# Performance work log

Measured on AMD Instinct MI355X. Metric: run time of the kernel, lower is better.

Reference implementation:

```python
import jax, jax.numpy as jnp
import numpy as np

B, S, HID = 2, 2048, 2048
NH, NKV, D = 32, 8, 64
M = 256          # FAVOR+ random features
CHUNK = 128      # causal chunk size
EPS = 1e-6


def setup_inputs():
    key = jax.random.key(0)
    ks = jax.random.split(key, 7)
    hidden_states = jax.random.normal(ks[0], (B, S, HID), jnp.float32)
    # RoPE tables (HF Llama style): [B, S, D]
    inv_freq = 1.0 / (10000.0 ** (jnp.arange(0, D, 2, dtype=jnp.float32) / D))
    freqs = jnp.arange(S, dtype=jnp.float32)[:, None] * inv_freq[None, :]   # [S, D/2]
    emb = jnp.concatenate([freqs, freqs], axis=-1)                          # [S, D]
    cos = jnp.broadcast_to(jnp.cos(emb)[None], (B, S, D)).astype(jnp.float32)
    sin = jnp.broadcast_to(jnp.sin(emb)[None], (B, S, D)).astype(jnp.float32)
    sc = 0.02
    Wq = jax.random.normal(ks[1], (NH * D, HID), jnp.float32) * sc
    Wk = jax.random.normal(ks[2], (NKV * D, HID), jnp.float32) * sc
    Wv = jax.random.normal(ks[3], (NKV * D, HID), jnp.float32) * sc
    Wo = jax.random.normal(ks[4], (HID, NH * D), jnp.float32) * sc
    proj = jax.random.normal(ks[5], (M, D), jnp.float32)  # FAVOR+ random projection
    return {"hidden_states": hidden_states, "cos": cos, "sin": sin,
            "Wq": Wq, "Wk": Wk, "Wv": Wv, "Wo": Wo, "proj": proj}


def rotate_half(x):
    x1, x2 = x[..., : x.shape[-1] // 2], x[..., x.shape[-1] // 2:]
    return jnp.concatenate([-x2, x1], axis=-1)


def favor_features(x, proj, is_query):
    # FAVOR+ positive softmax-kernel features: phi(x) = exp(Wx' - |x'|^2/2 - stab)/sqrt(m)
    dn = x.shape[-1] ** -0.25
    xn = x * dn                                            # data normalizer d^{-1/4}
    xp = jnp.einsum('bhsd,md->bhsm', xn, proj)             # [B,H,S,M]
    sq = 0.5 * jnp.sum(xn * xn, axis=-1, keepdims=True)
    if is_query:
        stab = jnp.max(xp, axis=-1, keepdims=True)
    else:
        stab = jnp.max(xp, axis=(-1, -2), keepdims=True)
    return (jnp.exp(xp - sq - stab) + EPS) / jnp.sqrt(jnp.asarray(M, xp.dtype))


def causal_linear_attention(phi_q, phi_k, v):
    # phi_q/phi_k: [B,H,S,M], v: [B,H,S,D]; causal chunked prefix formulation
    Bh, H, T, m = phi_q.shape
    d = v.shape[-1]
    nc = T // CHUNK
    qc = phi_q.reshape(Bh, H, nc, CHUNK, m)
    kc = phi_k.reshape(Bh, H, nc, CHUNK, m)
    vc = v.reshape(Bh, H, nc, CHUNK, d)
    # per-chunk KV state and key sums
    kv = jnp.einsum('bhscm,bhscd->bhsmd', kc, vc)          # [B,H,nc,M,D]
    kz = jnp.sum(kc, axis=3)                               # [B,H,nc,M]
    kv_pre = jnp.cumsum(kv, axis=2) - kv                   # exclusive prefix
    kz_pre = jnp.cumsum(kz, axis=2) - kz
    inter = jnp.einsum('bhscm,bhsmd->bhscd', qc, kv_pre)
    inter_z = jnp.einsum('bhscm,bhsm->bhsc', qc, kz_pre)
    # intra-chunk causal part
    mask = jnp.tril(jnp.ones((CHUNK, CHUNK), phi_q.dtype))
    scores = jnp.einsum('bhscm,bhstm->bhsct', qc, kc) * mask
    intra = jnp.einsum('bhsct,bhstd->bhscd', scores, vc)
    intra_z = jnp.sum(scores, axis=-1)
    out = (inter + intra) / (inter_z + intra_z + EPS)[..., None]
    return out.reshape(Bh, H, T, d)


def reference(hidden_states, cos, sin, Wq, Wk, Wv, Wo, proj):
    b, s, _ = hidden_states.shape
    q = (hidden_states @ Wq.T).reshape(b, s, NH, D).transpose(0, 2, 1, 3)   # [B,NH,S,D]
    k = (hidden_states @ Wk.T).reshape(b, s, NKV, D).transpose(0, 2, 1, 3)  # [B,NKV,S,D]
    v = (hidden_states @ Wv.T).reshape(b, s, NKV, D).transpose(0, 2, 1, 3)
    c, si = cos[:, None, :, :], sin[:, None, :, :]
    q = q * c + rotate_half(q) * si
    k = k * c + rotate_half(k) * si
    groups = NH // NKV
    k = jnp.repeat(k, groups, axis=1)
    v = jnp.repeat(v, groups, axis=1)
    phi_q = favor_features(q, proj, is_query=True)
    phi_k = favor_features(k, proj, is_query=False)
    attn = causal_linear_attention(phi_q, phi_k, v)                         # [B,NH,S,D]
    attn = attn.transpose(0, 2, 1, 3).reshape(b, s, NH * D)
    return attn @ Wo.T
```

## Files before the change

### kernel.cpp

```cpp
#include <hip/hip_runtime.h>
#include <hip/hip_bf16.h>

#define SEQ   2048
#define NHEAD 32
#define NKVH  8
#define DH    64
#define MFEAT 256
#define NCH   16
#define EPSF  1e-6f

typedef __hip_bfloat16 bf16;
typedef unsigned short u16;
typedef __attribute__((ext_vector_type(8))) short short8;
typedef __attribute__((ext_vector_type(4))) float f32x4;

__device__ __forceinline__ float b2f(bf16 x){ return __bfloat162float(x); }
__device__ __forceinline__ bf16  f2b(float x){ return __float2bfloat16(x); }
__device__ __forceinline__ u16   f2u(float x){ bf16 h = __float2bfloat16(x); return *reinterpret_cast<u16*>(&h); }

__device__ __forceinline__ bool probe_f32(const unsigned* __restrict__ p){
  return (p[0] & 0xFFFFu) == 0u;
}
__device__ __forceinline__ float loadIn(const void* __restrict__ ptr, size_t idx, bool f32){
  return f32 ? ((const float*)ptr)[idx] : b2f(((const bf16*)ptr)[idx]);
}

__device__ __forceinline__ void cp16(u16* lds, const u16* g){
  __builtin_amdgcn_global_load_lds((const __attribute__((address_space(1))) unsigned*)g,
      (__attribute__((address_space(3))) unsigned*)lds, 16, 0, 0);
}

#define MFMA16(a,b,c) __builtin_amdgcn_mfma_f32_16x16x32_bf16(a,b,c,0,0,0)

__global__ __launch_bounds__(256) void conv_kernel(const void* __restrict__ src,
    u16* __restrict__ dst, const unsigned* __restrict__ probe)
{
  const bool f32in = probe_f32(probe);
  size_t i = ((size_t)blockIdx.x*256 + threadIdx.x)*4;
  #pragma unroll
  for (int j=0;j<4;++j) dst[i+j] = f2u(loadIn(src, i+j, f32in));
}

__global__ __launch_bounds__(512) void gemm_mfma(const u16* __restrict__ A,
    const u16* __restrict__ W, float* __restrict__ oq, float* __restrict__ ok,
    float* __restrict__ ov, void* __restrict__ outAny, int K, int N, int mode,
    const void* __restrict__ cosg, const void* __restrict__ sing,
    const unsigned* __restrict__ probe)
{
  __shared__ __align__(16) u16 sA[3][16384];
  __shared__ __align__(16) u16 sB[3][8192];
  const int tid = threadIdx.x;
  const int lane = tid & 63, wave = tid >> 6;

  const int nbx = gridDim.x;
  const int nwg = nbx * gridDim.y;
  int id = blockIdx.y * nbx + blockIdx.x;
  int sw = id;
  if ((nwg & 7) == 0) sw = (id & 7) * (nwg >> 3) + (id >> 3);
  const int bx = sw % nbx, by = sw / nbx;
  const int c0 = bx*128, r0 = by*256;

  const int wm = wave >> 1, wn = wave & 1;
  f32x4 acc[4][4] = {};

  const int rl  = lane >> 3;
  const int swzE = ((lane & 7) ^ rl) << 3;
  const u16* gA = A + (size_t)(r0 + wave*8 + rl)*K + swzE;
  const u16* gB = W + (size_t)(c0 + wave*8 + rl)*K + swzE;
  const int aDst = wave*512;
  const int bDst = wave*512;

  const int rowA = (wm*64 + (lane&15))*64;
  const int rowB = (wn*64 + (lane&15))*64;
  const int colS = (((lane>>4)*8) ^ ((lane&7)<<3));

  const int nk = K >> 6;

  #define STAGE(buf, t) do { const int k0_ = (t)*64;                      \
    cp16(&sA[buf][aDst],         gA + k0_);                               \
    cp16(&sA[buf][aDst + 4096],  gA + (size_t)64*K  + k0_);               \
    cp16(&sA[buf][aDst + 8192],  gA + (size_t)128*K + k0_);               \
    cp16(&sA[buf][aDst + 12288], gA + (size_t)192*K + k0_);               \
    cp16(&sB[buf][bDst],         gB + k0_);                               \
    cp16(&sB[buf][bDst + 4096],  gB + (size_t)64*K  + k0_); } while(0)

  STAGE(0, 0);
  STAGE(1, 1);

  int cur = 0;
  for (int t = 0; t < nk; ++t) {
    if (t < nk-1) asm volatile("s_waitcnt vmcnt(6)" ::: "memory");
    else          asm volatile("s_waitcnt vmcnt(0)" ::: "memory");
    __builtin_amdgcn_s_barrier();
    __builtin_amdgcn_sched_barrier(0);

    if (t + 2 < nk) { int sb = cur + 2; if (sb >= 3) sb -= 3; STAGE(sb, t+2); }

    const u16* bA_ = sA[cur];
    const u16* bB_ = sB[cur];
    short8 af[4][2], bfv[4][2];
    #pragma unroll
    for (int mt=0;mt<4;++mt){
      af[mt][0] = *(const short8*)(bA_ + rowA + mt*1024 + colS);
      af[mt][1] = *(const short8*)(bA_ + rowA + mt*1024 + (colS^32));
    }
    #pragma unroll
    for (int nt=0;nt<4;++nt){
      bfv[nt][0] = *(const short8*)(bB_ + rowB + nt*1024 + colS);
      bfv[nt][1] = *(const short8*)(bB_ + rowB + nt*1024 + (colS^32));
    }
    __builtin_amdgcn_s_setprio(1);
    #pragma unroll
    for (int mt=0;mt<4;++mt)
      #pragma unroll
      for (int nt=0;nt<4;++nt){
        acc[mt][nt] = MFMA16(af[mt][0], bfv[nt][0], acc[mt][nt]);
        acc[mt][nt] = MFMA16(af[mt][1], bfv[nt][1], acc[mt][nt]);
      }
    __builtin_amdgcn_s_setprio(0);

    cur = (cur == 2) ? 0 : cur + 1;
  }
  #undef STAGE

  const int rbase = r0 + wm*64 + (lane>>4)*4;
  const int cbase = c0 + wn*64 + (lane&15);
  if (mode == 0) {
    const bool f32o = probe_f32(probe);
    #pragma unroll
    for (int mt=0;mt<4;++mt)
      #pragma unroll
      for (int nt=0;nt<4;++nt)
        #pragma unroll
        for (int rg=0;rg<4;++rg){
          int r = rbase + mt*16 + rg, c = cbase + nt*16;
          float v = acc[mt][nt][rg];
          if (f32o) ((float*)outAny)[(size_t)r*N + c] = v;
          else      ((u16*)outAny)[(size_t)r*N + c] = f2u(v);
        }
  } else {
    const bool f32in = probe_f32(probe);
    const float dn = 0.3535533905932738f;
    #pragma unroll
    for (int nt=0;nt<4;++nt){
      int cc = cbase + nt*16;
      float* dst; int H2, cl; bool isv = false;
      if (cc < 2048){ dst = oq; H2 = 32; cl = cc; }
      else if (cc < 2560){ dst = ok; H2 = 8; cl = cc - 2048; }
      else { dst = ov; H2 = 8; cl = cc - 2560; isv = true; }
      int hh = cl>>6, dd = cl&63;
      float sgn = (dd < 32) ? -1.f : 1.f;
      #pragma unroll
      for (int mt=0;mt<4;++mt)
        #pragma unroll
        for (int rg=0;rg<4;++rg){
          int r = rbase + mt*16 + rg;
          int bb = r>>11, s = r&2047;
          float v = acc[mt][nt][rg];
          if (!isv){
            float vp = acc[mt][nt^2][rg];
            size_t ci = ((size_t)bb*SEQ + s)*DH + dd;
            float cv = loadIn(cosg, ci, f32in);
            float sv = loadIn(sing, ci, f32in);
            v = (v*cv + sgn*vp*sv) * dn;
          }
          dst[(((size_t)bb*H2 + hh)*SEQ + s)*DH + dd] = v;
        }
    }
  }
}

__global__ __launch_bounds__(256) void phi_mfma(const float* __restrict__ xn,
    const u16* __restrict__ projb, float* __restrict__ rmaxk,
    const float* __restrict__ stabk, u16* __restrict__ phi, int mode)
{
  __shared__ __align__(16) u16 sA[64*80];
  __shared__ __align__(16) u16 sP[256*80];
  __shared__ float sq[64];
  const int tid = threadIdx.x, lane = tid & 63, wave = tid >> 6;
  const size_t row0 = (size_t)blockIdx.x * 64;

  #pragma unroll
  for (int l = 0; l < 8; ++l){
    int v8 = tid + l*256;
    int off = v8*8; int m = off>>6, d = off&63;
    *(short8*)&sP[m*80 + d] = ((const short8*)projb)[v8];
  }
  {
    int r = tid >> 2, qq = tid & 3;
    const float* src = xn + (row0 + r)*DH + qq*16;
    float s = 0.f;
    u16 tmp[16];
    #pragma unroll
    for (int i=0;i<16;i+=4){
      float4 v4 = *(const float4*)&src[i];
      s += v4.x*v4.x + v4.y*v4.y + v4.z*v4.z + v4.w*v4.w;
      tmp[i] = f2u(v4.x); tmp[i+1] = f2u(v4.y); tmp[i+2] = f2u(v4.z); tmp[i+3] = f2u(v4.w);
    }
    *(short8*)&sA[r*80 + qq*16]     = *(short8*)&tmp[0];
    *(short8*)&sA[r*80 + qq*16 + 8] = *(short8*)&tmp[8];
    s += __shfl_xor(s, 1, 64);
    s += __shfl_xor(s, 2, 64);
    if (qq == 0) sq[r] = 0.5f*s;
  }
  __syncthreads();

  f32x4 acc[16] = {};
  const u16* pA = &sA[(wave*16 + (lane&15))*80 + (lane>>4)*8];
  short8 af0 = *(const short8*)(pA);
  short8 af1 = *(const short8*)(pA + 32);
  #pragma unroll
  for (int nt=0; nt<16; ++nt){
    const u16* pB = &sP[(nt*16 + (lane&15))*80 + (lane>>4)*8];
    short8 b0 = *(const short8*)(pB);
    short8 b1 = *(const short8*)(pB + 32);
    acc[nt] = MFMA16(af0, b0, acc[nt]);
    acc[nt] = MFMA16(af1, b1, acc[nt]);
  }

  float mx[4];
  #pragma unroll
  for (int rg=0; rg<4; ++rg){
    float m = acc[0][rg];
    #pragma unroll
    for (int nt=1; nt<16; ++nt) m = fmaxf(m, acc[nt][rg]);
    m = fmaxf(m, __shfl_xor(m, 1, 64));
    m = fmaxf(m, __shfl_xor(m, 2, 64));
    m = fmaxf(m, __shfl_xor(m, 4, 64));
    m = fmaxf(m, __shfl_xor(m, 8, 64));
    mx[rg] = m;
  }
  const int rloc = wave*16 + (lane>>4)*4;
  if (mode == 1){
    if ((lane & 15) == 0){
      #pragma unroll
      for (int rg=0;rg<4;++rg) rmaxk[row0 + rloc + rg] = mx[rg];
    }
    return;
  }
  float stab[4];
  if (mode == 0){
    #pragma unroll
    for (int rg=0;rg<4;++rg) stab[rg] = mx[rg];
  } else {
    float s = stabk[row0 >> 11];
    #pragma unroll
    for (int rg=0;rg<4;++rg) stab[rg] = s;
  }
  float sqr[4];
  #pragma unroll
  for (int rg=0;rg<4;++rg) sqr[rg] = sq[rloc + rg];
  #pragma unroll
  for (int nt=0;nt<16;++nt){
    #pragma unroll
    for (int rg=0;rg<4;++rg){
      float val = (__expf(fminf(acc[nt][rg] - sqr[rg] - stab[rg], 0.f)) + EPSF) * 0.0625f;
      phi[(row0 + rloc + rg)*MFEAT + nt*16 + (lane&15)] = f2u(val);
    }
  }
}

__global__ void stab_reduce_kernel(const float* __restrict__ rmaxk, float* __restrict__ stabk){
  __shared__ float red[256];
  int bk = blockIdx.x;
  float mx = -1e30f;
  for (int i = threadIdx.x; i < SEQ; i += 256) mx = fmaxf(mx, rmaxk[(size_t)bk*SEQ + i]);
  red[threadIdx.x] = mx; __syncthreads();
  for (int off=128; off>0; off>>=1){
    if ((int)threadIdx.x < off) red[threadIdx.x] = fmaxf(red[threadIdx.x], red[threadIdx.x+off]);
    __syncthreads();
  }
  if (threadIdx.x==0) stabk[bk] = red[0];
}

__global__ __launch_bounds__(256) void kvchunk_kernel(const bf16* __restrict__ phik,
    const float* __restrict__ vbuf, float* __restrict__ kv, float* __restrict__ kz)
{
  int blk = blockIdx.x; int bk = blk >> 4, c = blk & 15;
  const bf16* Kc = phik + ((size_t)bk*SEQ + c*128)*MFEAT;
  const float* Vc = vbuf + ((size_t)bk*SEQ + c*128)*DH;
  __shared__ float sV[128*64];
  for (int l=0;l<32;++l){ int idx = threadIdx.x + l*256; sV[idx] = Vc[idx]; }
  __syncthreads();
  int m = threadIdx.x;
  float acc[64] = {}; float az = 0.f;
  for (int t=0;t<128;++t){
    float ph = b2f(Kc[(size_t)t*MFEAT + m]);
    az += ph;
    const float4* vr = (const float4*)&sV[t*64];
    #pragma unroll
    for (int d4=0; d4<16; ++d4){
      float4 v4 = vr[d4];
      acc[d4*4+0] += ph*v4.x; acc[d4*4+1] += ph*v4.y;
      acc[d4*4+2] += ph*v4.z; acc[d4*4+3] += ph*v4.w;
    }
  }
  float* out = kv + (size_t)blk*MFEAT*DH + (size_t)m*DH;
  #pragma unroll
  for (int d4=0; d4<16; ++d4)
    ((float4*)out)[d4] = make_float4(acc[d4*4],acc[d4*4+1],acc[d4*4+2],acc[d4*4+3]);
  kz[(size_t)blk*MFEAT + m] = az;
}

__global__ void scan_kernel(float* __restrict__ p, int inner, int nc, int total){
  int t = blockIdx.x*256 + threadIdx.x;
  if (t >= total) return;
  int outer = t / inner, rem = t - outer*inner;
  float* base = p + (size_t)outer*nc*inner + rem;
  float run = 0.f;
  for (int c=0;c<nc;++c){
    float v = base[(size_t)c*inner];
    base[(size_t)c*inner] = run;
    run += v;
  }
}

__global__ __launch_bounds__(256) void attn_mfma(
    const u16* __restrict__ phiq, const u16* __restrict__ phik,
    const float* __restrict__ vbuf, const float* __restrict__ kvp,
    const float* __restrict__ kzp, u16* __restrict__ attnout)
{
  __shared__ __align__(16) u16 smem[28288];
  __shared__ float sZ[128];
  const int tid = threadIdx.x, lane = tid & 63, wave = tid >> 6;
  const int blk = blockIdx.x;
  const int c = blk & 15, h = (blk >> 4) & 31, b = blk >> 9;
  const int kvh = h >> 2;
  const u16* Q   = phiq + (((size_t)(b*NHEAD+h)*SEQ) + c*128)*MFEAT;
  const u16* Kc  = phik + (((size_t)(b*NKVH+kvh)*SEQ) + c*128)*MFEAT;
  const float* Vc  = vbuf + (((size_t)(b*NKVH+kvh)*SEQ) + c*128)*DH;
  const float* KVp = kvp + ((size_t)((b*NKVH+kvh)*NCH + c))*MFEAT*DH;
  const float* KZp = kzp + ((size_t)((b*NKVH+kvh)*NCH + c))*MFEAT;

  u16* sQ   = smem;
  u16* sK   = smem + 4096;
  u16* sKVT = smem + 8192;
  u16* sP   = smem;
  u16* sVT  = smem + 17408;

  f32x4 accS[2][8] = {};
  f32x4 accO[2][5] = {};

  const int ch0 = wave*64 + lane, ch1 = 256 + wave*64 + lane;
  const u16* gQ0 = Q  + (ch0>>2)*MFEAT + (ch0&3)*8;
  const u16* gQ1 = Q  + (ch1>>2)*MFEAT + (ch1&3)*8;
  const u16* gK0 = Kc + (ch0>>2)*MFEAT + (ch0&3)*8;
  const u16* gK1 = Kc + (ch1>>2)*MFEAT + (ch1&3)*8;
  u16* lQ0 = &sQ[(wave*64)*8];  u16* lQ1 = &sQ[(256+wave*64)*8];
  u16* lK0 = &sK[(wave*64)*8];  u16* lK1 = &sK[(256+wave*64)*8];

  for (int k0 = 0; k0 < MFEAT; k0 += 32) {
    cp16(lQ0, gQ0 + k0); cp16(lQ1, gQ1 + k0);
    cp16(lK0, gK0 + k0); cp16(lK1, gK1 + k0);
    #pragma unroll
    for (int i=0;i<8;++i){
      int idx = tid + i*256;
      int m = idx >> 6, d = idx & 63;
      sKVT[d*72 + m] = f2u(KVp[(size_t)(k0+m)*DH + d]);
    }
    if (tid < 32) sKVT[64*72 + tid] = f2u(KZp[k0 + tid]);
    __syncthreads();
    short8 af0, af1;
    const u16* pQ = &sQ[(wave*32 + (lane&15))*32 + (lane>>4)*8];
    af0 = *(const short8*)(pQ);
    af1 = *(const short8*)(pQ + 512);
    #pragma unroll
    for (int nt=0;nt<8;++nt){
      short8 bk = *(const short8*)&sK[(nt*16 + (lane&15))*32 + (lane>>4)*8];
      accS[0][nt] = MFMA16(af0, bk, accS[0][nt]);
      accS[1][nt] = MFMA16(af1, bk, accS[1][nt]);
    }
    #pragma unroll
    for (int nt=0;nt<5;++nt){
      short8 bi = *(const short8*)&sKVT[(nt*16 + (lane&15))*72 + (lane>>4)*8];
      accO[0][nt] = MFMA16(af0, bi, accO[0][nt]);
      accO[1][nt] = MFMA16(af1, bi, accO[1][nt]);
    }
    __syncthreads();
  }

  #pragma unroll
  for (int mt=0;mt<2;++mt){
    int rowb = wave*32 + mt*16 + (lane>>4)*4;
    #pragma unroll
    for (int nt=0;nt<8;++nt){
      int col = nt*16 + (lane&15);
      #pragma unroll
      for (int rg=0;rg<4;++rg){
        int row = rowb + rg;
        float v = (col <= row) ? accS[mt][nt][rg] : 0.f;
        sP[row*136 + col] = f2u(v);
      }
    }
  }
  #pragma unroll
  for (int i=0;i<32;++i){
    int idx = tid + i*256;
    int t = idx >> 6, d = idx & 63;
    sVT[d*136 + t] = f2u(Vc[idx]);
  }
  if (tid < 128) sVT[64*136 + tid] = 0x3F80;
  __syncthreads();

  #pragma unroll
  for (int kc=0;kc<4;++kc){
    const u16* pP = &sP[(wave*32 + (lane&15))*136 + kc*32 + (lane>>4)*8];
    short8 pa0 = *(const short8*)(pP);
    short8 pa1 = *(const short8*)(pP + 16*136);
    #pragma unroll
    for (int nt=0;nt<5;++nt){
      short8 bv = *(const short8*)&sVT[(nt*16 + (lane&15))*136 + kc*32 + (lane>>4)*8];
      accO[0][nt] = MFMA16(pa0, bv, accO[0][nt]);
      accO[1][nt] = MFMA16(pa1, bv, accO[1][nt]);
    }
  }

  if ((lane & 15) == 0){
    #pragma unroll
    for (int mt=0;mt<2;++mt){
      int rowb = wave*32 + mt*16 + (lane>>4)*4;
      #pragma unroll
      for (int rg=0;rg<4;++rg) sZ[rowb + rg] = accO[mt][4][rg];
    }
  }
  __syncthreads();
  const int d0 = lane & 15;
  #pragma unroll
  for (int mt=0;mt<2;++mt){
    int rowb = wave*32 + mt*16 + (lane>>4)*4;
    #pragma unroll
    for (int rg=0;rg<4;++rg){
      int row = rowb + rg;
      float inv = 1.0f / (sZ[row] + EPSF);
      int sg = c*128 + row;
      size_t ob = (((size_t)b*SEQ + sg)*NHEAD + h)*DH;
      #pragma unroll
      for (int nt=0;nt<4;++nt)
        attnout[ob + nt*16 + d0] = f2u(accO[mt][nt][rg] * inv);
    }
  }
}

extern "C" void kernel_launch(void* const* d_in, const int* in_sizes, int n_in,
                              void* d_out, int out_size, void* d_ws, size_t ws_size,
                              hipStream_t stream)
{
  const void* hidden = d_in[0];
  const void* cosg   = d_in[1];
  const void* sing   = d_in[2];
  const void* Wq     = d_in[3];
  const void* Wk     = d_in[4];
  const void* Wv     = d_in[5];
  const void* Wo     = d_in[6];
  const void* proj   = d_in[7];
  const unsigned* probe = (const unsigned*)d_in[1];

  float* ws = (float*)d_ws;
  float* xnq   = ws;
  float* kv    = ws;
  float* kz    = ws + 4194304;
  float* rmaxk = ws + 4259840;
  float* stabk = ws + 4292608;
  float* xnk   = ws + 8388608;
  float* vbuf  = ws + 10485760;
  u16*   projb = (u16*) (ws + 12582912);
  bf16*  phiq  = (bf16*)(ws + 12591104);
  bf16*  phik  = (bf16*)(ws + 29368320);
  u16*   hb    = (u16*) (ws + 33562624);
  u16*   attn  = (u16*) (ws + 33562624);
  u16*   wqkv  = (u16*) (ws + 37756928);
  u16*   wob   = (u16*) (ws + 37756928);

  conv_kernel<<<8192, 256, 0, stream>>>(hidden, hb, probe);
  conv_kernel<<<4096, 256, 0, stream>>>(Wq, wqkv,           probe);
  conv_kernel<<<1024, 256, 0, stream>>>(Wk, wqkv + 4194304, probe);
  conv_kernel<<<1024, 256, 0, stream>>>(Wv, wqkv + 5242880, probe);
  conv_kernel<<<16,   256, 0, stream>>>(proj, projb, probe);

  gemm_mfma<<<dim3(24,16), 512, 0, stream>>>(hb, wqkv, xnq, xnk, vbuf, nullptr,
                                             2048, 3072, 1, cosg, sing, probe);
  conv_kernel<<<4096, 256, 0, stream>>>(Wo, wob, probe);

  phi_mfma<<<2048, 256, 0, stream>>>(xnq, projb, nullptr, nullptr, (u16*)phiq, 0);
  phi_mfma<<<512,  256, 0, stream>>>(xnk, projb, rmaxk, nullptr, nullptr, 1);
  stab_reduce_kernel<<<16, 256, 0, stream>>>(rmaxk, stabk);
  phi_mfma<<<512,  256, 0, stream>>>(xnk, projb, nullptr, stabk, (u16*)phik, 2);

  kvchunk_kernel<<<256, 256, 0, stream>>>(phik, vbuf, kv, kz);
  scan_kernel<<<1024, 256, 0, stream>>>(kv, MFEAT*DH, NCH, 16*MFEAT*DH);
  scan_kernel<<<16,   256, 0, stream>>>(kz, MFEAT,    NCH, 16*MFEAT);

  attn_mfma<<<1024, 256, 0, stream>>>((const u16*)phiq, (const u16*)phik,
                                      vbuf, kv, kz, attn);

  gemm_mfma<<<dim3(16,16), 512, 0, stream>>>(attn, wob, nullptr, nullptr, nullptr,
                                             d_out, 2048, 2048, 0, nullptr, nullptr, probe);
}
```

Baseline: 476.4 us.

## Split GEMM main loop into four quadrant phases interleaving LDS reads, global prefetch and MFMA

Restructures the projection GEMM inner loop into four 2x2 MFMA quadrant phases. LDS fragment loads and the async global-to-LDS prefetch for stage t+2 are spread across the phases, with block barriers between them. The aim is to overlap LDS reads and memory issue with matrix-core work and to lower peak fragment register pressure. It adds several workgroup barriers per K step, which may cost synchronisation overhead.

```diff
diff --git a/kernel.cpp b/kernel.cpp
--- a/kernel.cpp
+++ b/kernel.cpp
@@ -31,6 +31,7 @@
 }
 
 #define MFMA16(a,b,c) __builtin_amdgcn_mfma_f32_16x16x32_bf16(a,b,c,0,0,0)
+#define SBAR()  do { __builtin_amdgcn_s_barrier(); __builtin_amdgcn_sched_barrier(0); } while(0)
 
 __global__ __launch_bounds__(256) void conv_kernel(const void* __restrict__ src,
     u16* __restrict__ dst, const unsigned* __restrict__ probe)
@@ -76,7 +77,7 @@
 
   const int nk = K >> 6;
 
-  #define STAGE(buf, t) do { const int k0_ = (t)*64;                      \
+  #define STAGE_ALL(buf, t) do { const int k0_ = (t)*64;                  \
     cp16(&sA[buf][aDst],         gA + k0_);                               \
     cp16(&sA[buf][aDst + 4096],  gA + (size_t)64*K  + k0_);               \
     cp16(&sA[buf][aDst + 8192],  gA + (size_t)128*K + k0_);               \
@@ -84,44 +85,98 @@
     cp16(&sB[buf][bDst],         gB + k0_);                               \
     cp16(&sB[buf][bDst + 4096],  gB + (size_t)64*K  + k0_); } while(0)
 
-  STAGE(0, 0);
-  STAGE(1, 1);
+  STAGE_ALL(0, 0);
+  STAGE_ALL(1, 1);
 
   int cur = 0;
   for (int t = 0; t < nk; ++t) {
     if (t < nk-1) asm volatile("s_waitcnt vmcnt(6)" ::: "memory");
     else          asm volatile("s_waitcnt vmcnt(0)" ::: "memory");
-    __builtin_amdgcn_s_barrier();
-    __builtin_amdgcn_sched_barrier(0);
-
-    if (t + 2 < nk) { int sb = cur + 2; if (sb >= 3) sb -= 3; STAGE(sb, t+2); }
-
+    SBAR();
+
+    int sb = cur + 2; if (sb >= 3) sb -= 3;
+    const int k0s = (t + 2) * 64;
+    const bool st = (t + 2 < nk);
     const u16* bA_ = sA[cur];
     const u16* bB_ = sB[cur];
-    short8 af[4][2], bfv[4][2];
-    #pragma unroll
-    for (int mt=0;mt<4;++mt){
-      af[mt][0] = *(const short8*)(bA_ + rowA + mt*1024 + colS);
-      af[mt][1] = *(const short8*)(bA_ + rowA + mt*1024 + (colS^32));
-    }
-    #pragma unroll
-    for (int nt=0;nt<4;++nt){
-      bfv[nt][0] = *(const short8*)(bB_ + rowB + nt*1024 + colS);
-      bfv[nt][1] = *(const short8*)(bB_ + rowB + nt*1024 + (colS^32));
-    }
+
+    short8 a01[2][2], a23[2][2], b01[2][2], b23[2][2];
+
+    #pragma unroll
+    for (int mt=0;mt<2;++mt){
+      a01[mt][0] = *(const short8*)(bA_ + rowA + mt*1024 + colS);
+      a01[mt][1] = *(const short8*)(bA_ + rowA + mt*1024 + (colS^32));
+    }
+    #pragma unroll
+    for (int nt=0;nt<2;++nt){
+      b01[nt][0] = *(const short8*)(bB_ + rowB + nt*1024 + colS);
+      b01[nt][1] = *(const short8*)(bB_ + rowB + nt*1024 + (colS^32));
+    }
+    if (st){ cp16(&sA[sb][aDst], gA + k0s);
+             cp16(&sA[sb][aDst + 4096], gA + (size_t)64*K + k0s); }
+    SBAR();
     __builtin_amdgcn_s_setprio(1);
     #pragma unroll
-    for (int mt=0;mt<4;++mt)
-      #pragma unroll
-      for (int nt=0;nt<4;++nt){
-        acc[mt][nt] = MFMA16(af[mt][0], bfv[nt][0], acc[mt][nt]);
-        acc[mt][nt] = MFMA16(af[mt][1], bfv[nt][1], acc[mt][nt]);
+    for (int mt=0;mt<2;++mt)
+      #pragma unroll
+      for (int nt=0;nt<2;++nt){
+        acc[mt][nt] = MFMA16(a01[mt][0], b01[nt][0], acc[mt][nt]);
+        acc[mt][nt] = MFMA16(a01[mt][1], b01[nt][1], acc[mt][nt]);
       }
     __builtin_amdgcn_s_setprio(0);
+    SBAR();
+
+    #pragma unroll
+    for (int nt=0;nt<2;++nt){
+      b23[nt][0] = *(const short8*)(bB_ + rowB + (nt+2)*1024 + colS);
+      b23[nt][1] = *(const short8*)(bB_ + rowB + (nt+2)*1024 + (colS^32));
+    }
+    if (st){ cp16(&sA[sb][aDst + 8192],  gA + (size_t)128*K + k0s);
+             cp16(&sA[sb][aDst + 12288], gA + (size_t)192*K + k0s); }
+    SBAR();
+    __builtin_amdgcn_s_setprio(1);
+    #pragma unroll
+    for (int mt=0;mt<2;++mt)
+      #pragma unroll
+      for (int nt=0;nt<2;++nt){
+        acc[mt][nt+2] = MFMA16(a01[mt][0], b23[nt][0], acc[mt][nt+2]);
+        acc[mt][nt+2] = MFMA16(a01[mt][1], b23[nt][1], acc[mt][nt+2]);
+      }
+    __builtin_amdgcn_s_setprio(0);
+    SBAR();
+
+    #pragma unroll
+    for (int mt=0;mt<2;++mt){
+      a23[mt][0] = *(const short8*)(bA_ + rowA + (mt+2)*1024 + colS);
+      a23[mt][1] = *(const short8*)(bA_ + rowA + (mt+2)*1024 + (colS^32));
+    }
+    if (st){ cp16(&sB[sb][bDst], gB + k0s);
+             cp16(&sB[sb][bDst + 4096], gB + (size_t)64*K + k0s); }
+    SBAR();
+    __builtin_amdgcn_s_setprio(1);
+    #pragma unroll
+    for (int mt=0;mt<2;++mt)
+      #pragma unroll
+      for (int nt=0;nt<2;++nt){
+        acc[mt+2][nt+2] = MFMA16(a23[mt][0], b23[nt][0], acc[mt+2][nt+2]);
+        acc[mt+2][nt+2] = MFMA16(a23[mt][1], b23[nt][1], acc[mt+2][nt+2]);
+      }
+    __builtin_amdgcn_s_setprio(0);
+    SBAR();
+
+    __builtin_amdgcn_s_setprio(1);
+    #pragma unroll
+    for (int mt=0;mt<2;++mt)
+      #pragma unroll
+      for (int nt=0;nt<2;++nt){
+        acc[mt+2][nt] = MFMA16(a23[mt][0], b01[nt][0], acc[mt+2][nt]);
+        acc[mt+2][nt] = MFMA16(a23[mt][1], b01[nt][1], acc[mt+2][nt]);
+      }
+    __builtin_amdgcn_s_setprio(0);
 
     cur = (cur == 2) ? 0 : cur + 1;
   }
-  #undef STAGE
+  #undef STAGE_ALL
 
   const int rbase = r0 + wm*64 + (lane>>4)*4;
   const int cbase = c0 + wn*64 + (lane&15);
```

New measurement: 462.4 us. 2.9% less time.
